# Kernel optimization log

Hardware: AMD Instinct MI355X
Metric: run time of the kernel (lower is better)

The kernel has to match this reference:

```python
import jax, jax.numpy as jnp
import numpy as np

B, D, H, W = 2, 256, 64, 64
NH = 4
EPS = 1e-5


def _ln(x, g, b):
    # LayerNorm over channel dim of NCHW tensor (matches permute->LN(C)->permute)
    mu = jnp.mean(x, axis=1, keepdims=True)
    var = jnp.mean((x - mu) ** 2, axis=1, keepdims=True)
    xn = (x - mu) * jax.lax.rsqrt(var + EPS)
    return xn * g[None, :, None, None] + b[None, :, None, None]


def _conv1x1(x, w, b):
    # w: (out_c, in_c)
    return jnp.einsum('bchw,oc->bohw', x, w) + b[None, :, None, None]


def _dwconv3x3(x, w, b):
    # depthwise 3x3, w: (C, 1, 3, 3)
    y = jax.lax.conv_general_dilated(
        x, w, window_strides=(1, 1), padding='SAME',
        dimension_numbers=('NCHW', 'OIHW', 'NCHW'), feature_group_count=D)
    return y + b[None, :, None, None]


def setup_inputs() -> dict:
    key = jax.random.key(0)
    ks = jax.random.split(key, 12)
    sc = 0.02

    def n(k, shape):
        return jax.random.normal(k, shape, dtype=jnp.float32) * sc

    return {
        'image_embedding': jax.random.normal(ks[0], (B, D, H, W), dtype=jnp.float32),
        'guide': jax.random.normal(ks[1], (B, D, H, W), dtype=jnp.float32),
        'ln1_g': jnp.ones((D,), jnp.float32), 'ln1_b': jnp.zeros((D,), jnp.float32),
        'ln2_g': jnp.ones((D,), jnp.float32), 'ln2_b': jnp.zeros((D,), jnp.float32),
        'qw1': n(ks[2], (D, D)), 'qb1': jnp.zeros((D,), jnp.float32),
        'qw2': n(ks[3], (D, 1, 3, 3)), 'qb2': jnp.zeros((D,), jnp.float32),
        'kw1': n(ks[4], (D, D)), 'kb1': jnp.zeros((D,), jnp.float32),
        'kw2': n(ks[5], (D, 1, 3, 3)), 'kb2': jnp.zeros((D,), jnp.float32),
        'vw1': n(ks[6], (D, D)), 'vb1': jnp.zeros((D,), jnp.float32),
        'vw2': n(ks[7], (D, 1, 3, 3)), 'vb2': jnp.zeros((D,), jnp.float32),
        'ow': n(ks[8], (D, D)), 'ob': jnp.zeros((D,), jnp.float32),
    }


def reference(image_embedding, guide, ln1_g, ln1_b, ln2_g, ln2_b,
              qw1, qb1, qw2, qb2, kw1, kb1, kw2, kb2,
              vw1, vb1, vw2, vb2, ow, ob):
    residual = image_embedding
    x = _ln(image_embedding, ln1_g, ln1_b)
    g = _ln(guide, ln2_g, ln2_b)

    q = _dwconv3x3(_conv1x1(x, qw1, qb1), qw2, qb2)
    k = _dwconv3x3(_conv1x1(g, kw1, kb1), kw2, kb2)
    v = _dwconv3x3(_conv1x1(g, vw1, vb1), vw2, vb2)

    hd = D // NH
    scale = hd ** -0.5

    def to_heads(t):  # (B,C,H,W) -> (B, NH, HW, hd)
        return t.reshape(B, NH, hd, H * W).transpose(0, 1, 3, 2)

    q = to_heads(q) * scale
    k = to_heads(k)
    v = to_heads(v)

    attn = jax.nn.softmax(jnp.einsum('bhnd,bhmd->bhnm', q, k), axis=-1)
    out = jnp.einsum('bhnm,bhmd->bhnd', attn, v)
    out = out.transpose(0, 1, 3, 2).reshape(B, D, H, W)
    out = _conv1x1(out, ow, ob)
    return residual + out
```

## Files before the change

### kernel.cpp

```cpp
#include <hip/hip_runtime.h>
#include <cstdint>
#include <cstddef>

typedef unsigned short u16;
typedef unsigned int u32;
typedef __attribute__((ext_vector_type(8))) short short8;
typedef __attribute__((ext_vector_type(4))) float f32x4;
typedef __attribute__((ext_vector_type(16))) float f32x16;
typedef __attribute__((ext_vector_type(2))) unsigned int u32x2;

#define CD 256
#define HWD 4096
#define NHD 4
#define HDD 64
#define NSPLIT 4

static __device__ __forceinline__ u16 f2b(float f) {
    u32 u = __builtin_bit_cast(u32, f);
    return (u16)((u + 0x7fffu + ((u >> 16) & 1u)) >> 16);
}
static __device__ __forceinline__ float b2f(u16 h) {
    return __builtin_bit_cast(float, (u32)h << 16);
}
static __device__ __forceinline__ u32 pk2(float a, float b) {
    return (u32)f2b(a) | ((u32)f2b(b) << 16);
}
static __device__ __forceinline__ float fexp2(float x) {
#if __has_builtin(__builtin_amdgcn_exp2f)
    return __builtin_amdgcn_exp2f(x);
#else
    return __expf(x * 0.69314718056f);
#endif
}
static __device__ __forceinline__ u32 cvtpk(float lo, float hi) {
    u32 r;
    asm("v_cvt_pk_bf16_f32 %0, %1, %2" : "=v"(r) : "v"(lo), "v"(hi));
    return r;
}
static __device__ __forceinline__ u32x2 plswap(u32 a, u32 b) {
    return __builtin_amdgcn_permlane32_swap(a, b, false, false);
}
static __device__ __forceinline__ void async16(const void* g, void* l) {
    __builtin_amdgcn_global_load_lds(
        (const __attribute__((address_space(1))) unsigned int*)g,
        (__attribute__((address_space(3))) unsigned int*)l,
        16, 0, 0);
}

__global__ __launch_bounds__(256) void ln_transpose(
    const float* __restrict__ x0, const float* __restrict__ x1,
    const float* __restrict__ g0, const float* __restrict__ b0,
    const float* __restrict__ g1, const float* __restrict__ b1,
    const float* __restrict__ qw1, const float* __restrict__ kw1,
    const float* __restrict__ vw1, const float* __restrict__ ow,
    u16* __restrict__ out0, u16* __restrict__ out1, u16* __restrict__ wbf)
{
    int bid = blockIdx.x;
    int tid = threadIdx.x;

    if (bid >= 512) {
        int base = (bid - 512) * 8192 + tid * 32;
        int which = base >> 16;
        int off = base & 65535;
        const float* s = (which == 0) ? qw1 : (which == 1) ? kw1
                       : (which == 2) ? vw1 : ow;
        s += off;
        u16* d = wbf + (size_t)which * 65536 + off;
        #pragma unroll
        for (int j = 0; j < 4; ++j) {
            float4 a = ((const float4*)s)[2 * j];
            float4 b = ((const float4*)s)[2 * j + 1];
            uint4 o;
            o.x = pk2(a.x, a.y); o.y = pk2(a.z, a.w);
            o.z = pk2(b.x, b.y); o.w = pk2(b.z, b.w);
            ((uint4*)d)[j] = o;
        }
        return;
    }

    int t = bid >> 8, b = (bid >> 7) & 1, p0 = (bid & 127) << 5;
    const float* x = t ? x1 : x0;
    const float* g = t ? g1 : g0;
    const float* bb = t ? b1 : b0;
    u16* out = t ? out1 : out0;

    int tx = tid & 31, ty = tid >> 5;
    const float* xb = x + (size_t)b * CD * HWD + p0 + tx;

    __shared__ float red[2][8][32];
    __shared__ u16 T[256][33];

    float s = 0.f, sq = 0.f;
    #pragma unroll 8
    for (int i = 0; i < 32; ++i) {
        float v = xb[(size_t)(ty * 32 + i) * HWD];
        s += v; sq += v * v;
    }
    red[0][ty][tx] = s; red[1][ty][tx] = sq;
    __syncthreads();
    float st = 0.f, sqt = 0.f;
    #pragma unroll
    for (int j = 0; j < 8; ++j) { st += red[0][j][tx]; sqt += red[1][j][tx]; }
    float mean = st * (1.f / 256.f);
    float var = sqt * (1.f / 256.f) - mean * mean;
    float rstd = rsqrtf(var + 1e-5f);

    #pragma unroll 8
    for (int i = 0; i < 32; ++i) {
        int c = ty * 32 + i;
        float v = (xb[(size_t)c * HWD] - mean) * rstd * g[c] + bb[c];
        T[c][tx] = f2b(v);
    }
    __syncthreads();

    #pragma unroll
    for (int pass = 0; pass < 4; ++pass) {
        int idx = pass * 256 + tid;
        int p = idx >> 5, cs = (idx & 31) * 8;
        u16 tmp[8];
        #pragma unroll
        for (int j = 0; j < 8; ++j) tmp[j] = T[cs + j][p];
        *(uint4*)&out[((size_t)b * HWD + p0 + p) * CD + cs] = *(const uint4*)tmp;
    }
}

__global__ __launch_bounds__(256) void qkv_gemm(
    const u16* __restrict__ xT, const u16* __restrict__ gT,
    const u16* __restrict__ Wbf,
    const float* __restrict__ qb1, const float* __restrict__ kb1,
    const float* __restrict__ vb1,
    u16* __restrict__ q1, u16* __restrict__ k1, u16* __restrict__ v1)
{
    int z = blockIdx.z;
    int mm = z >> 1, b = z & 1;
    const u16* X    = (mm == 0) ? xT : gT;
    const u16* W    = Wbf + (size_t)mm * 65536;
    const float* Bi = (mm == 0) ? qb1 : (mm == 1) ? kb1 : vb1;
    u16* Y          = (mm == 0) ? q1 : (mm == 1) ? k1 : v1;

    int n0 = blockIdx.x * 128;
    int p0 = blockIdx.y * 64;

    __shared__ u16 As[64][40];
    __shared__ u16 Bs[128][40];

    int tid = threadIdx.x;
    int lane = tid & 63, w = tid >> 6;
    int wm = w >> 1, wn = w & 1;
    int l15 = lane & 15, quad = lane >> 4;

    f32x4 acc[2][4];
    #pragma unroll
    for (int mi = 0; mi < 2; ++mi)
        #pragma unroll
        for (int nj = 0; nj < 4; ++nj)
            acc[mi][nj] = (f32x4){0.f, 0.f, 0.f, 0.f};

    const u16* Xb = X + (size_t)b * HWD * CD;

    int arow = tid >> 2, aseg = (tid & 3) * 8;
    const u16* agp = Xb + (size_t)(p0 + arow) * CD + aseg;
    int brow = tid >> 1, bkh = (tid & 1) * 16;
    const u16* wgp = W + (size_t)(n0 + brow) * CD + bkh;

    uint4 ra = *(const uint4*)(agp);
    uint4 rb0 = ((const uint4*)wgp)[0], rb1 = ((const uint4*)wgp)[1];

    for (int kt = 0; kt < 8; ++kt) {
        __syncthreads();
        *(uint4*)&As[arow][aseg] = ra;
        *(uint4*)&Bs[brow][bkh] = rb0;
        *(uint4*)&Bs[brow][bkh + 8] = rb1;
        if (kt < 7) {
            ra = *(const uint4*)(agp + (kt + 1) * 32);
            const u16* wg2 = wgp + (kt + 1) * 32;
            rb0 = ((const uint4*)wg2)[0]; rb1 = ((const uint4*)wg2)[1];
        }
        __syncthreads();

        short8 af[2], bf[4];
        #pragma unroll
        for (int mi = 0; mi < 2; ++mi)
            af[mi] = *(const short8*)&As[wm * 32 + mi * 16 + l15][quad * 8];
        #pragma unroll
        for (int nj = 0; nj < 4; ++nj)
            bf[nj] = *(const short8*)&Bs[wn * 64 + nj * 16 + l15][quad * 8];
        #pragma unroll
        for (int mi = 0; mi < 2; ++mi)
            #pragma unroll
            for (int nj = 0; nj < 4; ++nj)
                acc[mi][nj] = __builtin_amdgcn_mfma_f32_16x16x32_bf16(
                    af[mi], bf[nj], acc[mi][nj], 0, 0, 0);
    }

    u16* Yb = Y + (size_t)b * HWD * CD;
    float bias[4];
    #pragma unroll
    for (int nj = 0; nj < 4; ++nj)
        bias[nj] = Bi[n0 + wn * 64 + nj * 16 + l15];
    #pragma unroll
    for (int mi = 0; mi < 2; ++mi) {
        #pragma unroll
        for (int r = 0; r < 4; ++r) {
            int p = p0 + wm * 32 + mi * 16 + quad * 4 + r;
            #pragma unroll
            for (int nj = 0; nj < 4; ++nj) {
                int ch = n0 + wn * 64 + nj * 16 + l15;
                Yb[(size_t)p * CD + ch] = f2b(acc[mi][nj][r] + bias[nj]);
            }
        }
    }
}

__global__ __launch_bounds__(256) void dwconv_nc(
    const u16* __restrict__ q1, const u16* __restrict__ k1, const u16* __restrict__ v1,
    const float* __restrict__ qw2, const float* __restrict__ qb2,
    const float* __restrict__ kw2, const float* __restrict__ kb2,
    const float* __restrict__ vw2, const float* __restrict__ vb2,
    u16* __restrict__ Q, u16* __restrict__ K, u16* __restrict__ Vt)
{
    int bid = blockIdx.x;
    int which = bid >> 9;
    int b = (bid >> 8) & 1;
    int p0 = (bid & 255) * 16;

    const u16* in = ((which == 0) ? q1 : (which == 1) ? k1 : v1) + (size_t)b * HWD * CD;
    const float* wsrc = (which == 0) ? qw2 : (which == 1) ? kw2 : vw2;
    const float* bsrc = (which == 0) ? qb2 : (which == 1) ? kb2 : vb2;
    float oscale = (which == 0) ? 0.18033688011112042f : 1.0f;

    int c = threadIdx.x;
    float w9[9];
    #pragma unroll
    for (int j = 0; j < 9; ++j) w9[j] = wsrc[c * 9 + j];
    float bias = bsrc[c];

    int h = p0 >> 6, w0 = p0 & 63;

    float accv[16];
    #pragma unroll
    for (int pi = 0; pi < 16; ++pi) accv[pi] = bias;

    #pragma unroll
    for (int dh = 0; dh < 3; ++dh) {
        int hh = h + dh - 1;
        if (hh < 0 || hh >= 64) continue;
        const u16* rp = in + ((size_t)hh * 64) * CD + c;
        float r[18];
        r[0] = (w0 > 0) ? b2f(rp[(size_t)(w0 - 1) * CD]) : 0.f;
        #pragma unroll
        for (int j = 1; j <= 16; ++j)
            r[j] = b2f(rp[(size_t)(w0 - 1 + j) * CD]);
        r[17] = (w0 < 48) ? b2f(rp[(size_t)(w0 + 16) * CD]) : 0.f;

        float wa = w9[dh * 3 + 0], wb = w9[dh * 3 + 1], wc = w9[dh * 3 + 2];
        #pragma unroll
        for (int pi = 0; pi < 16; ++pi)
            accv[pi] += wa * r[pi] + wb * r[pi + 1] + wc * r[pi + 2];
    }

    if (which == 2) {
        u32 w8[8];
        #pragma unroll
        for (int j = 0; j < 8; ++j) w8[j] = pk2(accv[2 * j], accv[2 * j + 1]);
        uint4* dst = (uint4*)(Vt + ((size_t)(b * CD + c)) * HWD + p0);
        dst[0] = make_uint4(w8[0], w8[1], w8[2], w8[3]);
        dst[1] = make_uint4(w8[4], w8[5], w8[6], w8[7]);
    } else {
        u16* out = ((which == 0) ? Q : K) + (size_t)b * HWD * CD;
        #pragma unroll
        for (int pi = 0; pi < 16; ++pi)
            out[(size_t)(p0 + pi) * CD + c] = f2b(accv[pi] * oscale);
    }
}

__global__ __launch_bounds__(256, 4) void attn_kernel(
    const u16* __restrict__ Q, const u16* __restrict__ K,
    const u16* __restrict__ Vt, u16* __restrict__ Opart,
    float* __restrict__ Psum)
{
    int qt = blockIdx.x;
    int bh = blockIdx.y;
    int ks = blockIdx.z;
    int b = bh >> 2, nh = bh & 3;

    __shared__ u16 Ks_[2][64 * 64];
    __shared__ u16 Vs_[2][64 * 64];

    int tid = threadIdx.x;
    int lane = tid & 63, w = tid >> 6;
    int l31 = lane & 31, h = lane >> 5;
    int sw = l31 & 7;

    const u16* Qb = Q + ((size_t)b * HWD) * CD + nh * 64;
    const u16* Kb = K + ((size_t)b * HWD) * CD + nh * 64;
    const u16* Vb = Vt + ((size_t)bh * HDD) * HWD;

    int q0 = qt * 128 + w * 32;

    short8 qf[4];
    #pragma unroll
    for (int si = 0; si < 4; ++si)
        qf[si] = *(const short8*)(Qb + (size_t)(q0 + l31) * CD + si * 16 + h * 8);

    int rr = lane >> 3;
    int gseg = (lane & 7) ^ rr;
    const u16* kgb = Kb + (size_t)(ks * 1024 + w * 16 + rr) * CD + gseg * 8;
    const u16* vgb = Vb + (size_t)(w * 16 + rr) * HWD + ks * 1024 + gseg * 8;

    f32x16 acc[2];
    #pragma unroll
    for (int db = 0; db < 2; ++db)
        #pragma unroll
        for (int r = 0; r < 16; ++r) acc[db][r] = 0.f;
    float psum = 0.f;

    #pragma unroll
    for (int j = 0; j < 2; ++j) {
        async16(kgb + (size_t)(j * 8) * CD, &Ks_[0][(w * 16 + j * 8) * 64]);
        async16(vgb + (size_t)(j * 8) * HWD, &Vs_[0][(w * 16 + j * 8) * 64]);
    }

    for (int it = 0; it < 16; ++it) {
        int cur = it & 1;
        __syncthreads();
        if (it + 1 < 16) {
            int nxt = cur ^ 1;
            #pragma unroll
            for (int j = 0; j < 2; ++j) {
                async16(kgb + (size_t)((it + 1) * 64 + j * 8) * CD,
                        &Ks_[nxt][(w * 16 + j * 8) * 64]);
                async16(vgb + (size_t)(j * 8) * HWD + (it + 1) * 64,
                        &Vs_[nxt][(w * 16 + j * 8) * 64]);
            }
        }

        #pragma unroll
        for (int kb = 0; kb < 2; ++kb) {
            short8 kf[4];
            #pragma unroll
            for (int si = 0; si < 4; ++si)
                kf[si] = *(const short8*)&Ks_[cur][(kb * 32 + l31) * 64 +
                                                   (((si * 2 + h) ^ sw) << 3)];
            f32x16 st;
            #pragma unroll
            for (int r = 0; r < 16; ++r) st[r] = 0.f;
            __builtin_amdgcn_s_setprio(1);
            #pragma unroll
            for (int si = 0; si < 4; ++si)
                st = __builtin_amdgcn_mfma_f32_32x32x16_bf16(
                    kf[si], qf[si], st, 0, 0, 0);
            __builtin_amdgcn_s_setprio(0);

            float e[16];
            #pragma unroll
            for (int r = 0; r < 16; ++r) e[r] = fexp2(st[r]);
            #pragma unroll
            for (int r = 0; r < 16; r += 4)
                psum += (e[r] + e[r + 1]) + (e[r + 2] + e[r + 3]);

            u32 wv[8];
            #pragma unroll
            for (int m = 0; m < 8; ++m) wv[m] = cvtpk(e[2 * m], e[2 * m + 1]);
            u32x2 s02 = plswap(wv[0], wv[2]);
            u32x2 s13 = plswap(wv[1], wv[3]);
            u32x2 s46 = plswap(wv[4], wv[6]);
            u32x2 s57 = plswap(wv[5], wv[7]);
            union { u32 u[4]; short8 s8; } p0_, p1_;
            p0_.u[0] = s02.x; p0_.u[1] = s13.x; p0_.u[2] = s02.y; p0_.u[3] = s13.y;
            p1_.u[0] = s46.x; p1_.u[1] = s57.x; p1_.u[2] = s46.y; p1_.u[3] = s57.y;

            #pragma unroll
            for (int db = 0; db < 2; ++db) {
                short8 vf0 = *(const short8*)&Vs_[cur][(db * 32 + l31) * 64 +
                                 ((((kb * 2 + 0) * 2 + h) ^ sw) << 3)];
                short8 vf1 = *(const short8*)&Vs_[cur][(db * 32 + l31) * 64 +
                                 ((((kb * 2 + 1) * 2 + h) ^ sw) << 3)];
                __builtin_amdgcn_s_setprio(1);
                acc[db] = __builtin_amdgcn_mfma_f32_32x32x16_bf16(
                    p0_.s8, vf0, acc[db], 0, 0, 0);
                acc[db] = __builtin_amdgcn_mfma_f32_32x32x16_bf16(
                    p1_.s8, vf1, acc[db], 0, 0, 0);
                __builtin_amdgcn_s_setprio(0);
            }
        }
    }

    u16* Ob = Opart + (((size_t)ks * 8 + bh) * HWD) * HDD;
    #pragma unroll
    for (int db = 0; db < 2; ++db)
        #pragma unroll
        for (int r = 0; r < 16; ++r) {
            int n = q0 + (r & 3) + 8 * (r >> 2) + 4 * h;
            Ob[(size_t)n * HDD + db * 32 + l31] = f2b(acc[db][r]);
        }

    float s = psum + __shfl_xor(psum, 32);
    float* Pb = Psum + ((size_t)ks * 8 + bh) * HWD + q0;
    if (lane < 32) Pb[lane] = s;
}

__global__ __launch_bounds__(256) void out_gemm(
    const u16* __restrict__ Wo, const float* __restrict__ Bi,
    const u16* __restrict__ Opart, const float* __restrict__ Psum,
    const float* __restrict__ residual, float* __restrict__ out)
{
    int b = blockIdx.z;
    int m0 = blockIdx.y * 64;
    int n0 = blockIdx.x * 64;

    __shared__ u16 As[64][40];
    __shared__ u16 Bs[64][40];

    int tid = threadIdx.x;
    int lane = tid & 63, w = tid >> 6;
    int wm = w >> 1, wn = w & 1;
    int l15 = lane & 15, quad = lane >> 4;

    f32x4 acc[2][2];
    #pragma unroll
    for (int mi = 0; mi < 2; ++mi)
        #pragma unroll
        for (int nj = 0; nj < 2; ++nj)
            acc[mi][nj] = (f32x4){0.f, 0.f, 0.f, 0.f};

    int arow = tid >> 2, aseg = (tid & 3) * 8;
    const u16* wgp = Wo + (size_t)(m0 + arow) * CD + aseg;
    int brow = tid >> 2, bseg = (tid & 3) * 8;
    int pn = n0 + brow;

    uint4 ra = *(const uint4*)wgp;

    uint4 ro[NSPLIT]; float rinv;
    {
        int c = bseg;
        int bh = b * 4 + (c >> 6), d0 = c & 63;
        float p = 0.f;
        #pragma unroll
        for (int s = 0; s < NSPLIT; ++s) {
            ro[s] = *(const uint4*)&Opart[(((size_t)s * 8 + bh) * HWD + pn) * HDD + d0];
            p += Psum[((size_t)s * 8 + bh) * HWD + pn];
        }
        rinv = 1.f / p;
    }

    for (int kt = 0; kt < 8; ++kt) {
        __syncthreads();
        *(uint4*)&As[arow][aseg] = ra;
        {
            float v[8];
            #pragma unroll
            for (int j = 0; j < 8; ++j) v[j] = 0.f;
            #pragma unroll
            for (int s = 0; s < NSPLIT; ++s) {
                u16 t[8];
                *(uint4*)t = ro[s];
                #pragma unroll
                for (int j = 0; j < 8; ++j) v[j] += b2f(t[j]);
            }
            uint4 bb;
            bb.x = pk2(v[0] * rinv, v[1] * rinv);
            bb.y = pk2(v[2] * rinv, v[3] * rinv);
            bb.z = pk2(v[4] * rinv, v[5] * rinv);
            bb.w = pk2(v[6] * rinv, v[7] * rinv);
            *(uint4*)&Bs[brow][bseg] = bb;
        }
        if (kt < 7) {
            ra = *(const uint4*)(wgp + (kt + 1) * 32);
            int c = (kt + 1) * 32 + bseg;
            int bh = b * 4 + (c >> 6), d0 = c & 63;
            float p = 0.f;
            #pragma unroll
            for (int s = 0; s < NSPLIT; ++s) {
                ro[s] = *(const uint4*)&Opart[(((size_t)s * 8 + bh) * HWD + pn) * HDD + d0];
                p += Psum[((size_t)s * 8 + bh) * HWD + pn];
            }
            rinv = 1.f / p;
        }
        __syncthreads();

        short8 af[2], bf[2];
        #pragma unroll
        for (int mi = 0; mi < 2; ++mi)
            af[mi] = *(const short8*)&As[wm * 32 + mi * 16 + l15][quad * 8];
        #pragma unroll
        for (int nj = 0; nj < 2; ++nj)
            bf[nj] = *(const short8*)&Bs[wn * 32 + nj * 16 + l15][quad * 8];
        #pragma unroll
        for (int mi = 0; mi < 2; ++mi)
            #pragma unroll
            for (int nj = 0; nj < 2; ++nj)
                acc[mi][nj] = __builtin_amdgcn_mfma_f32_16x16x32_bf16(
                    af[mi], bf[nj], acc[mi][nj], 0, 0, 0);
    }

    #pragma unroll
    for (int mi = 0; mi < 2; ++mi) {
        int mb = m0 + wm * 32 + mi * 16 + quad * 4;
        #pragma unroll
        for (int r = 0; r < 4; ++r) {
            float bias = Bi[mb + r];
            const float* res = residual + (size_t)(b * CD + mb + r) * HWD;
            float* o = out + (size_t)(b * CD + mb + r) * HWD;
            #pragma unroll
            for (int nj = 0; nj < 2; ++nj) {
                int n = n0 + wn * 32 + nj * 16 + l15;
                o[n] = acc[mi][nj][r] + bias + res[n];
            }
        }
    }
}

extern "C" void kernel_launch(void* const* d_in, const int* in_sizes, int n_in,
                              void* d_out, int out_size, void* d_ws, size_t ws_size,
                              hipStream_t stream) {
    (void)in_sizes; (void)n_in; (void)out_size; (void)ws_size;

    const float* image = (const float*)d_in[0];
    const float* guide = (const float*)d_in[1];
    const float* ln1_g = (const float*)d_in[2];
    const float* ln1_b = (const float*)d_in[3];
    const float* ln2_g = (const float*)d_in[4];
    const float* ln2_b = (const float*)d_in[5];
    const float* qw1 = (const float*)d_in[6];
    const float* qb1 = (const float*)d_in[7];
    const float* qw2 = (const float*)d_in[8];
    const float* qb2 = (const float*)d_in[9];
    const float* kw1 = (const float*)d_in[10];
    const float* kb1 = (const float*)d_in[11];
    const float* kw2 = (const float*)d_in[12];
    const float* kb2 = (const float*)d_in[13];
    const float* vw1 = (const float*)d_in[14];
    const float* vb1 = (const float*)d_in[15];
    const float* vw2 = (const float*)d_in[16];
    const float* vb2 = (const float*)d_in[17];
    const float* ow  = (const float*)d_in[18];
    const float* ob  = (const float*)d_in[19];
    float* out = (float*)d_out;

    char* ws = (char*)d_ws;
    u16* xT    = (u16*)(ws + (size_t)0  * (1 << 20));
    u16* gT    = (u16*)(ws + (size_t)4  * (1 << 20));
    u16* q1    = (u16*)(ws + (size_t)8  * (1 << 20));
    u16* k1    = (u16*)(ws + (size_t)12 * (1 << 20));
    u16* v1    = (u16*)(ws + (size_t)16 * (1 << 20));
    u16* Qh    = (u16*)(ws + (size_t)20 * (1 << 20));
    u16* Kh    = (u16*)(ws + (size_t)24 * (1 << 20));
    u16* Vt    = (u16*)(ws + (size_t)28 * (1 << 20));
    u16*   Opart = (u16*)(ws + (size_t)0  * (1 << 20));
    float* Psum  = (float*)(ws + (size_t)18 * (1 << 20));
    u16*   Wbf   = (u16*)(ws + (size_t)33 * (1 << 20));

    ln_transpose<<<dim3(544), dim3(256), 0, stream>>>(
        image, guide, ln1_g, ln1_b, ln2_g, ln2_b,
        qw1, kw1, vw1, ow, xT, gT, Wbf);

    qkv_gemm<<<dim3(2, 64, 6), dim3(256), 0, stream>>>(
        xT, gT, Wbf, qb1, kb1, vb1, q1, k1, v1);

    dwconv_nc<<<dim3(1536), dim3(256), 0, stream>>>(
        q1, k1, v1, qw2, qb2, kw2, kb2, vw2, vb2, Qh, Kh, Vt);

    attn_kernel<<<dim3(32, 8, NSPLIT), dim3(256), 0, stream>>>(Qh, Kh, Vt, Opart, Psum);

    out_gemm<<<dim3(64, 4, 2), dim3(256), 0, stream>>>(
        Wbf + (size_t)3 * 65536, ob, Opart, Psum, image, out);
}
```

Before: 176.0 us.

## Split attention combine into its own kernel and widen GEMM K-tiles to 64

Adds a combine_kernel that reduces the split-K attention partials and normalizes by the summed softmax denominators into a bf16 buffer. out_gemm no longer redoes that reduction for every output-channel block; it now reads the combined buffer directly. Both qkv_gemm and out_gemm move from K-tiles of 32 to 64, halving the number of shared-memory stages and barriers. The cost is one extra kernel launch, an extra global write and read of the combined tensor, and larger LDS tiles.

```diff
diff --git a/kernel.cpp b/kernel.cpp
--- a/kernel.cpp
+++ b/kernel.cpp
@@ -141,8 +141,8 @@
     int n0 = blockIdx.x * 128;
     int p0 = blockIdx.y * 64;
 
-    __shared__ u16 As[64][40];
-    __shared__ u16 Bs[128][40];
+    __shared__ u16 As[64][72];
+    __shared__ u16 Bs[128][72];
 
     int tid = threadIdx.x;
     int lane = tid & 63, w = tid >> 6;
@@ -158,39 +158,48 @@
 
     const u16* Xb = X + (size_t)b * HWD * CD;
 
-    int arow = tid >> 2, aseg = (tid & 3) * 8;
+    int arow = tid >> 2, aseg = (tid & 3) * 16;
     const u16* agp = Xb + (size_t)(p0 + arow) * CD + aseg;
-    int brow = tid >> 1, bkh = (tid & 1) * 16;
+    int brow = tid >> 1, bkh = (tid & 1) * 32;
     const u16* wgp = W + (size_t)(n0 + brow) * CD + bkh;
 
-    uint4 ra = *(const uint4*)(agp);
+    uint4 ra0 = ((const uint4*)agp)[0], ra1 = ((const uint4*)agp)[1];
     uint4 rb0 = ((const uint4*)wgp)[0], rb1 = ((const uint4*)wgp)[1];
-
-    for (int kt = 0; kt < 8; ++kt) {
+    uint4 rb2 = ((const uint4*)wgp)[2], rb3 = ((const uint4*)wgp)[3];
+
+    for (int kt = 0; kt < 4; ++kt) {
         __syncthreads();
-        *(uint4*)&As[arow][aseg] = ra;
+        *(uint4*)&As[arow][aseg] = ra0;
+        *(uint4*)&As[arow][aseg + 8] = ra1;
         *(uint4*)&Bs[brow][bkh] = rb0;
         *(uint4*)&Bs[brow][bkh + 8] = rb1;
-        if (kt < 7) {
-            ra = *(const uint4*)(agp + (kt + 1) * 32);
-            const u16* wg2 = wgp + (kt + 1) * 32;
+        *(uint4*)&Bs[brow][bkh + 16] = rb2;
+        *(uint4*)&Bs[brow][bkh + 24] = rb3;
+        if (kt < 3) {
+            const u16* ag2 = agp + (kt + 1) * 64;
+            ra0 = ((const uint4*)ag2)[0]; ra1 = ((const uint4*)ag2)[1];
+            const u16* wg2 = wgp + (kt + 1) * 64;
             rb0 = ((const uint4*)wg2)[0]; rb1 = ((const uint4*)wg2)[1];
+            rb2 = ((const uint4*)wg2)[2]; rb3 = ((const uint4*)wg2)[3];
         }
         __syncthreads();
 
-        short8 af[2], bf[4];
-        #pragma unroll
-        for (int mi = 0; mi < 2; ++mi)
-            af[mi] = *(const short8*)&As[wm * 32 + mi * 16 + l15][quad * 8];
-        #pragma unroll
-        for (int nj = 0; nj < 4; ++nj)
-            bf[nj] = *(const short8*)&Bs[wn * 64 + nj * 16 + l15][quad * 8];
-        #pragma unroll
-        for (int mi = 0; mi < 2; ++mi)
+        #pragma unroll
+        for (int kk = 0; kk < 2; ++kk) {
+            short8 af[2], bf[4];
+            #pragma unroll
+            for (int mi = 0; mi < 2; ++mi)
+                af[mi] = *(const short8*)&As[wm * 32 + mi * 16 + l15][kk * 32 + quad * 8];
             #pragma unroll
             for (int nj = 0; nj < 4; ++nj)
-                acc[mi][nj] = __builtin_amdgcn_mfma_f32_16x16x32_bf16(
-                    af[mi], bf[nj], acc[mi][nj], 0, 0, 0);
+                bf[nj] = *(const short8*)&Bs[wn * 64 + nj * 16 + l15][kk * 32 + quad * 8];
+            #pragma unroll
+            for (int mi = 0; mi < 2; ++mi)
+                #pragma unroll
+                for (int nj = 0; nj < 4; ++nj)
+                    acc[mi][nj] = __builtin_amdgcn_mfma_f32_16x16x32_bf16(
+                        af[mi], bf[nj], acc[mi][nj], 0, 0, 0);
+        }
     }
 
     u16* Yb = Y + (size_t)b * HWD * CD;
@@ -400,17 +409,51 @@
     if (lane < 32) Pb[lane] = s;
 }
 
+__global__ __launch_bounds__(256) void combine_kernel(
+    const u16* __restrict__ Opart, const float* __restrict__ Psum,
+    u16* __restrict__ Oc)
+{
+    int tid = blockIdx.x * 256 + threadIdx.x;
+    int pn = tid >> 5;
+    int c0 = (tid & 31) * 8;
+    int b = pn >> 12;
+    int p = pn & 4095;
+    int bh = b * 4 + (c0 >> 6);
+    int d0 = c0 & 63;
+
+    float v[8];
+    #pragma unroll
+    for (int j = 0; j < 8; ++j) v[j] = 0.f;
+    float ps = 0.f;
+    #pragma unroll
+    for (int s = 0; s < NSPLIT; ++s) {
+        uint4 t4 = *(const uint4*)&Opart[(((size_t)s * 8 + bh) * HWD + p) * HDD + d0];
+        u16 t[8];
+        *(uint4*)t = t4;
+        #pragma unroll
+        for (int j = 0; j < 8; ++j) v[j] += b2f(t[j]);
+        ps += Psum[((size_t)s * 8 + bh) * HWD + p];
+    }
+    float rinv = 1.f / ps;
+    uint4 o;
+    o.x = pk2(v[0] * rinv, v[1] * rinv);
+    o.y = pk2(v[2] * rinv, v[3] * rinv);
+    o.z = pk2(v[4] * rinv, v[5] * rinv);
+    o.w = pk2(v[6] * rinv, v[7] * rinv);
+    *(uint4*)&Oc[(size_t)pn * CD + c0] = o;
+}
+
 __global__ __launch_bounds__(256) void out_gemm(
     const u16* __restrict__ Wo, const float* __restrict__ Bi,
-    const u16* __restrict__ Opart, const float* __restrict__ Psum,
+    const u16* __restrict__ Oc,
     const float* __restrict__ residual, float* __restrict__ out)
 {
     int b = blockIdx.z;
     int m0 = blockIdx.y * 64;
     int n0 = blockIdx.x * 64;
 
-    __shared__ u16 As[64][40];
-    __shared__ u16 Bs[64][40];
+    __shared__ u16 As[64][72];
+    __shared__ u16 Bs[64][72];
 
     int tid = threadIdx.x;
     int lane = tid & 63, w = tid >> 6;
@@ -424,74 +467,43 @@
         for (int nj = 0; nj < 2; ++nj)
             acc[mi][nj] = (f32x4){0.f, 0.f, 0.f, 0.f};
 
-    int arow = tid >> 2, aseg = (tid & 3) * 8;
+    int arow = tid >> 2, aseg = (tid & 3) * 16;
     const u16* wgp = Wo + (size_t)(m0 + arow) * CD + aseg;
-    int brow = tid >> 2, bseg = (tid & 3) * 8;
-    int pn = n0 + brow;
-
-    uint4 ra = *(const uint4*)wgp;
-
-    uint4 ro[NSPLIT]; float rinv;
-    {
-        int c = bseg;
-        int bh = b * 4 + (c >> 6), d0 = c & 63;
-        float p = 0.f;
-        #pragma unroll
-        for (int s = 0; s < NSPLIT; ++s) {
-            ro[s] = *(const uint4*)&Opart[(((size_t)s * 8 + bh) * HWD + pn) * HDD + d0];
-            p += Psum[((size_t)s * 8 + bh) * HWD + pn];
-        }
-        rinv = 1.f / p;
-    }
-
-    for (int kt = 0; kt < 8; ++kt) {
+    const u16* bgp = Oc + ((size_t)b * HWD + n0 + arow) * CD + aseg;
+
+    uint4 ra0 = ((const uint4*)wgp)[0], ra1 = ((const uint4*)wgp)[1];
+    uint4 rb0 = ((const uint4*)bgp)[0], rb1 = ((const uint4*)bgp)[1];
+
+    for (int kt = 0; kt < 4; ++kt) {
         __syncthreads();
-        *(uint4*)&As[arow][aseg] = ra;
-        {
-            float v[8];
-            #pragma unroll
-            for (int j = 0; j < 8; ++j) v[j] = 0.f;
-            #pragma unroll
-            for (int s = 0; s < NSPLIT; ++s) {
-                u16 t[8];
-                *(uint4*)t = ro[s];
+        *(uint4*)&As[arow][aseg] = ra0;
+        *(uint4*)&As[arow][aseg + 8] = ra1;
+        *(uint4*)&Bs[arow][aseg] = rb0;
+        *(uint4*)&Bs[arow][aseg + 8] = rb1;
+        if (kt < 3) {
+            const u16* wg2 = wgp + (kt + 1) * 64;
+            ra0 = ((const uint4*)wg2)[0]; ra1 = ((const uint4*)wg2)[1];
+            const u16* bg2 = bgp + (kt + 1) * 64;
+            rb0 = ((const uint4*)bg2)[0]; rb1 = ((const uint4*)bg2)[1];
+        }
+        __syncthreads();
+
+        #pragma unroll
+        for (int kk = 0; kk < 2; ++kk) {
+            short8 af[2], bf[2];
+            #pragma unroll
+            for (int mi = 0; mi < 2; ++mi)
+                af[mi] = *(const short8*)&As[wm * 32 + mi * 16 + l15][kk * 32 + quad * 8];
+            #pragma unroll
+            for (int nj = 0; nj < 2; ++nj)
+                bf[nj] = *(const short8*)&Bs[wn * 32 + nj * 16 + l15][kk * 32 + quad * 8];
+            #pragma unroll
+            for (int mi = 0; mi < 2; ++mi)
                 #pragma unroll
-                for (int j = 0; j < 8; ++j) v[j] += b2f(t[j]);
-            }
-            uint4 bb;
-            bb.x = pk2(v[0] * rinv, v[1] * rinv);
-            bb.y = pk2(v[2] * rinv, v[3] * rinv);
-            bb.z = pk2(v[4] * rinv, v[5] * rinv);
-            bb.w = pk2(v[6] * rinv, v[7] * rinv);
-            *(uint4*)&Bs[brow][bseg] = bb;
-        }
-        if (kt < 7) {
-            ra = *(const uint4*)(wgp + (kt + 1) * 32);
-            int c = (kt + 1) * 32 + bseg;
-            int bh = b * 4 + (c >> 6), d0 = c & 63;
-            float p = 0.f;
-            #pragma unroll
-            for (int s = 0; s < NSPLIT; ++s) {
-                ro[s] = *(const uint4*)&Opart[(((size_t)s * 8 + bh) * HWD + pn) * HDD + d0];
-                p += Psum[((size_t)s * 8 + bh) * HWD + pn];
-            }
-            rinv = 1.f / p;
-        }
-        __syncthreads();
-
-        short8 af[2], bf[2];
-        #pragma unroll
-        for (int mi = 0; mi < 2; ++mi)
-            af[mi] = *(const short8*)&As[wm * 32 + mi * 16 + l15][quad * 8];
-        #pragma unroll
-        for (int nj = 0; nj < 2; ++nj)
-            bf[nj] = *(const short8*)&Bs[wn * 32 + nj * 16 + l15][quad * 8];
-        #pragma unroll
-        for (int mi = 0; mi < 2; ++mi)
-            #pragma unroll
-            for (int nj = 0; nj < 2; ++nj)
-                acc[mi][nj] = __builtin_amdgcn_mfma_f32_16x16x32_bf16(
-                    af[mi], bf[nj], acc[mi][nj], 0, 0, 0);
+                for (int nj = 0; nj < 2; ++nj)
+                    acc[mi][nj] = __builtin_amdgcn_mfma_f32_16x16x32_bf16(
+                        af[mi], bf[nj], acc[mi][nj], 0, 0, 0);
+        }
     }
 
     #pragma unroll
@@ -550,6 +562,7 @@
     u16*   Opart = (u16*)(ws + (size_t)0  * (1 << 20));
     float* Psum  = (float*)(ws + (size_t)18 * (1 << 20));
     u16*   Wbf   = (u16*)(ws + (size_t)33 * (1 << 20));
+    u16*   Ocomb = (u16*)(ws + (size_t)36 * (1 << 20));
 
     ln_transpose<<<dim3(544), dim3(256), 0, stream>>>(
         image, guide, ln1_g, ln1_b, ln2_g, ln2_b,
@@ -563,6 +576,8 @@
 
     attn_kernel<<<dim3(32, 8, NSPLIT), dim3(256), 0, stream>>>(Qh, Kh, Vt, Opart, Psum);
 
+    combine_kernel<<<dim3(1024), dim3(256), 0, stream>>>(Opart, Psum, Ocomb);
+
     out_gemm<<<dim3(64, 4, 2), dim3(256), 0, stream>>>(
-        Wbf + (size_t)3 * 65536, ob, Opart, Psum, image, out);
-}
+        Wbf + (size_t)3 * 65536, ob, Ocomb, image, out);
+}
```

Result: no change. 176.7 us (+0.4%).
